# Kernel optimization log

Hardware: AMD Instinct MI355X
Metric: run time of the kernel (lower is better)

Reference implementation:

```python
import jax, jax.numpy as jnp
import numpy as np

N = 100000   # num nodes
E = 1200000  # num edges
D = 64       # embedding dim
K = 3        # propagation hops (alpha has K+1 entries)


def setup_inputs() -> dict:
    key = jax.random.key(0)
    k1, k2, k3 = jax.random.split(key, 3)
    edge_index = jax.random.randint(k1, (2, E), 0, N, dtype=jnp.int64)
    weight = jax.random.normal(k2, (N, D), dtype=jnp.float32)
    alpha = jax.random.uniform(k3, (K + 1,), dtype=jnp.float32)
    return {"edge_index": edge_index, "weight": weight, "alpha": alpha}


def reference(edge_index, weight, alpha):
    row = edge_index[0]  # source j
    col = edge_index[1]  # target i
    # symmetric normalization: in-degree over col, deg^-1/2 with inf -> 0
    deg = jax.ops.segment_sum(jnp.ones((E,), dtype=weight.dtype), col, num_segments=N)
    dinv = jnp.where(deg == 0, 0.0, deg ** -0.5)
    edge_w = dinv[row] * dinv[col]  # [E]

    out = weight * alpha[0]
    x = weight
    for k in range(1, K + 1):
        # gather-scale-scatter propagation hop
        msg = edge_w[:, None] * x[row]                      # [E, D]
        x = jax.ops.segment_sum(msg, col, num_segments=N)   # [N, D]
        out = out + x * alpha[k]

    # per-edge link scores: dot(out[src], out[dst])
    return jnp.sum(out[row] * out[col], axis=-1)  # [E]
```

## Files before the change

kernel.cpp:

```cpp
#include <hip/hip_runtime.h>
#include <hip/hip_bf16.h>

#define GN 100000
#define GE 1200000
#define GD 64
#define NG 256
#define CPG 391
#define CAP 6144


__global__ void detect_kernel(const void* __restrict__ w,
                              const void* __restrict__ edge,
                              int* __restrict__ flags, int* __restrict__ gcount) {
    __shared__ int s_badw, s_edgenz;
    if (threadIdx.x == 0) { s_badw = 0; s_edgenz = 0; }
    gcount[threadIdx.x] = 0;
    __syncthreads();
    const unsigned short* wh = (const unsigned short*)w;
    const unsigned int*   ei = (const unsigned int*)edge;
    int badw = 0, edgenz = 0;
    for (int i = threadIdx.x; i < 4096; i += 256) {
        unsigned int bits = ((unsigned int)wh[i]) << 16;
        float v = __uint_as_float(bits);
        if (!(fabsf(v) <= 100.0f)) badw = 1;
        if ((i & 1) == 1 && ei[i] != 0u) edgenz = 1;
    }
    if (badw)   atomicOr(&s_badw, 1);
    if (edgenz) atomicOr(&s_edgenz, 1);
    __syncthreads();
    if (threadIdx.x == 0) {
        flags[0] = s_badw ? 0 : 1;
        flags[1] = s_edgenz ? 0 : 1;
    }
}

__device__ __forceinline__ int ld_row(const int* __restrict__ edge, int e, int e64) {
    return e64 ? edge[2 * (size_t)e] : edge[e];
}
__device__ __forceinline__ int ld_col(const int* __restrict__ edge, int e, int e64) {
    return e64 ? edge[2 * ((size_t)GE + (size_t)e)] : edge[(size_t)GE + (size_t)e];
}
__device__ __forceinline__ float ld_f(const void* __restrict__ p, size_t i, int bf16f) {
    if (bf16f) return __bfloat162float(((const __hip_bfloat16*)p)[i]);
    return ((const float*)p)[i];
}

__device__ __forceinline__ float bf_lo(unsigned u) { return __uint_as_float(u << 16); }
__device__ __forceinline__ float bf_hi(unsigned u) { return __uint_as_float(u & 0xFFFF0000u); }
__device__ __forceinline__ unsigned bf16bits(float f) {
    __hip_bfloat16 h = __float2bfloat16(f);
    unsigned short s;
    __builtin_memcpy(&s, &h, 2);
    return (unsigned)s;
}

__global__ void p1init_kernel(const int* __restrict__ edge, const int* __restrict__ flags,
                              int* __restrict__ gcount, unsigned* __restrict__ bucket,
                              int E, int chunk,
                              const void* __restrict__ w, const void* __restrict__ alpha,
                              __hip_bfloat16* __restrict__ X,
                              __hip_bfloat16* __restrict__ OUT, int nd) {
    if (blockIdx.x < NG) {
        __shared__ int cnt[NG];
        __shared__ int base[NG];
        int t = threadIdx.x;
        int e64 = flags[1];
        cnt[t] = 0;
        __syncthreads();
        int lo = blockIdx.x * chunk;
        int hiE = min(lo + chunk, E);
        for (int e = lo + t; e < hiE; e += 256) {
            int c = ld_col(edge, e, e64);
            int r = ld_row(edge, e, e64);
            if ((unsigned)c < (unsigned)GN && (unsigned)r < (unsigned)GN)
                atomicAdd(&cnt[c / CPG], 1);
        }
        __syncthreads();
        int cv = cnt[t];
        base[t] = (cv > 0) ? atomicAdd(&gcount[t], cv) : 0;
        __syncthreads();
        cnt[t] = 0;
        __syncthreads();
        for (int e = lo + t; e < hiE; e += 256) {
            int c = ld_col(edge, e, e64);
            int r = ld_row(edge, e, e64);
            if ((unsigned)c < (unsigned)GN && (unsigned)r < (unsigned)GN) {
                int g = c / CPG;
                int idx = base[g] + atomicAdd(&cnt[g], 1);
                if (idx < CAP)
                    bucket[(size_t)g * CAP + idx] = ((unsigned)(c - g * CPG) << 17) | (unsigned)r;
            }
        }
    } else {
        int bid = blockIdx.x - NG;
        int i = 4 * (bid * 256 + (int)threadIdx.x);
        int wbf = flags[0];
        if (i < nd) {
            float a0 = ld_f(alpha, 0, wbf);
            float v0 = ld_f(w, i + 0, wbf);
            float v1 = ld_f(w, i + 1, wbf);
            float v2 = ld_f(w, i + 2, wbf);
            float v3 = ld_f(w, i + 3, wbf);
            uint2 xq;
            xq.x = (bf16bits(v1) << 16) | bf16bits(v0);
            xq.y = (bf16bits(v3) << 16) | bf16bits(v2);
            *(uint2*)(X + i) = xq;
            uint2 oq;
            oq.x = (bf16bits(a0 * v1) << 16) | bf16bits(a0 * v0);
            oq.y = (bf16bits(a0 * v3) << 16) | bf16bits(a0 * v2);
            *(uint2*)(OUT + i) = oq;
        }
    }
}

__global__ void p2_kernel(const unsigned* __restrict__ bucket, const int* __restrict__ gcount,
                          int* __restrict__ rowptr, float* __restrict__ dinv,
                          int* __restrict__ csr) {
    int g = blockIdx.x;
    int t = threadIdx.x;
    __shared__ int gs[NG];
    __shared__ int hist[512];
    __shared__ int s[512];
    int gv = gcount[t]; if (gv > CAP) gv = CAP;
    gs[t] = gv;
    hist[t] = 0; hist[t + 256] = 0;
    __syncthreads();
    for (int off = 1; off < NG; off <<= 1) {
        int u = (t >= off) ? gs[t - off] : 0;
        __syncthreads();
        gs[t] += u;
        __syncthreads();
    }
    int mg = gcount[g]; if (mg > CAP) mg = CAP;
    int gb = gs[g] - mg;
    int m = mg;
    const unsigned* bk = bucket + (size_t)g * CAP;
    for (int idx = t; idx < m; idx += 256)
        atomicAdd(&hist[bk[idx] >> 17], 1);
    __syncthreads();
    int h0 = hist[t], h1 = hist[t + 256];
    s[t] = h0; s[t + 256] = h1;
    __syncthreads();
    for (int off = 1; off < 512; off <<= 1) {
        int v0 = (t >= off) ? s[t - off] : 0;
        int v1 = (t + 256 >= off) ? s[t + 256 - off] : 0;
        __syncthreads();
        s[t] += v0; s[t + 256] += v1;
        __syncthreads();
    }
    int col0 = g * CPG + t;
    int col1 = col0 + 256;
    if (col0 < GN) {
        rowptr[col0] = gb + s[t];
        dinv[col0] = (h0 > 0) ? rsqrtf((float)h0) : 0.0f;
    }
    if (t + 256 < CPG && col1 < GN) {
        rowptr[col1] = gb + s[t + 256];
        dinv[col1] = (h1 > 0) ? rsqrtf((float)h1) : 0.0f;
    }
    __syncthreads();
    hist[t] = s[t] - h0;
    hist[t + 256] = s[t + 256] - h1;
    __syncthreads();
    for (int idx = t; idx < m; idx += 256) {
        unsigned u = bk[idx];
        int cl = u >> 17;
        int r  = (int)(u & 0x1FFFFu);
        int pos = gb + atomicAdd(&hist[cl], 1);
        csr[pos] = r;
    }
}

__global__ void gather_kernel(const __hip_bfloat16* __restrict__ X,
                              __hip_bfloat16* __restrict__ Y,
                              __hip_bfloat16* __restrict__ OUT,
                              const int* __restrict__ rowptr, const int* __restrict__ csr,
                              const float* __restrict__ dinv,
                              const void* __restrict__ alpha, const int* __restrict__ flags,
                              int k, int store_y, int N) {
    int t = blockIdx.x * blockDim.x + threadIdx.x;
    int node = __builtin_amdgcn_readfirstlane(t >> 6);
    if (node >= N) return;
    int lane = t & 63;
    int h = lane >> 4;
    int i = lane & 15;
    int beg = node ? rowptr[node - 1] : 0;
    int end = rowptr[node];
    float dc = dinv[node];
    float a = ld_f(alpha, k, flags[0]);
    size_t obase = (size_t)node * GD + 4 * i;
    uint2 uo = *(const uint2*)(OUT + obase);
    float f0 = 0.0f, f1 = 0.0f, f2 = 0.0f, f3 = 0.0f;
    for (int j = beg; j < end; j += 16) {
        int i0 = j + 0 + h;  int i1 = j + 4 + h;
        int i2 = j + 8 + h;  int i3 = j + 12 + h;
        int last = end - 1;
        int r0 = csr[min(i0, last)];
        int r1 = csr[min(i1, last)];
        int r2 = csr[min(i2, last)];
        int r3 = csr[min(i3, last)];
        float w0 = (i0 < end) ? dinv[r0] : 0.0f;
        float w1 = (i1 < end) ? dinv[r1] : 0.0f;
        float w2 = (i2 < end) ? dinv[r2] : 0.0f;
        float w3 = (i3 < end) ? dinv[r3] : 0.0f;
        uint2 u0 = *(const uint2*)(X + (size_t)r0 * GD + 4 * i);
        uint2 u1 = *(const uint2*)(X + (size_t)r1 * GD + 4 * i);
        uint2 u2 = *(const uint2*)(X + (size_t)r2 * GD + 4 * i);
        uint2 u3 = *(const uint2*)(X + (size_t)r3 * GD + 4 * i);
        f0 = fmaf(w0, bf_lo(u0.x), f0); f1 = fmaf(w0, bf_hi(u0.x), f1);
        f2 = fmaf(w0, bf_lo(u0.y), f2); f3 = fmaf(w0, bf_hi(u0.y), f3);
        f0 = fmaf(w1, bf_lo(u1.x), f0); f1 = fmaf(w1, bf_hi(u1.x), f1);
        f2 = fmaf(w1, bf_lo(u1.y), f2); f3 = fmaf(w1, bf_hi(u1.y), f3);
        f0 = fmaf(w2, bf_lo(u2.x), f0); f1 = fmaf(w2, bf_hi(u2.x), f1);
        f2 = fmaf(w2, bf_lo(u2.y), f2); f3 = fmaf(w2, bf_hi(u2.y), f3);
        f0 = fmaf(w3, bf_lo(u3.x), f0); f1 = fmaf(w3, bf_hi(u3.x), f1);
        f2 = fmaf(w3, bf_lo(u3.y), f2); f3 = fmaf(w3, bf_hi(u3.y), f3);
    }
    f0 += __shfl_xor(f0, 16, 64); f0 += __shfl_xor(f0, 32, 64);
    f1 += __shfl_xor(f1, 16, 64); f1 += __shfl_xor(f1, 32, 64);
    f2 += __shfl_xor(f2, 16, 64); f2 += __shfl_xor(f2, 32, 64);
    f3 += __shfl_xor(f3, 16, 64); f3 += __shfl_xor(f3, 32, 64);
    f0 *= dc; f1 *= dc; f2 *= dc; f3 *= dc;
    if (h == 0) {
        if (store_y) {
            uint2 p;
            p.x = (bf16bits(f1) << 16) | bf16bits(f0);
            p.y = (bf16bits(f3) << 16) | bf16bits(f2);
            *(uint2*)(Y + obase) = p;
        }
        float o0 = fmaf(a, f0, bf_lo(uo.x));
        float o1 = fmaf(a, f1, bf_hi(uo.x));
        float o2 = fmaf(a, f2, bf_lo(uo.y));
        float o3 = fmaf(a, f3, bf_hi(uo.y));
        uint2 q;
        q.x = (bf16bits(o1) << 16) | bf16bits(o0);
        q.y = (bf16bits(o3) << 16) | bf16bits(o2);
        *(uint2*)(OUT + obase) = q;
    }
}

__device__ __forceinline__ float dot2_bf16(unsigned ua, unsigned ub) {
    return fmaf(bf_lo(ua), bf_lo(ub), bf_hi(ua) * bf_hi(ub));
}

__global__ void dot_kernel(const __hip_bfloat16* __restrict__ OUT,
                           const int* __restrict__ edge, const int* __restrict__ flags,
                           void* __restrict__ res, int E) {
    int t = blockIdx.x * blockDim.x + threadIdx.x;
    int e = t >> 2;
    int sub = t & 3;
    if (e >= E) return;
    int e64 = flags[1];
    int wbf = flags[0];
    int r = ld_row(edge, e, e64);
    int c = ld_col(edge, e, e64);
    float p = 0.0f;
    if ((unsigned)r < (unsigned)GN && (unsigned)c < (unsigned)GN) {
        const uint4* pa = (const uint4*)(OUT + (size_t)r * GD + sub * 16);
        const uint4* pb = (const uint4*)(OUT + (size_t)c * GD + sub * 16);
        uint4 a0 = pa[0], a1 = pa[1];
        uint4 b0 = pb[0], b1 = pb[1];
        p = ((dot2_bf16(a0.x, b0.x) + dot2_bf16(a0.y, b0.y)) +
             (dot2_bf16(a0.z, b0.z) + dot2_bf16(a0.w, b0.w))) +
            ((dot2_bf16(a1.x, b1.x) + dot2_bf16(a1.y, b1.y)) +
             (dot2_bf16(a1.z, b1.z) + dot2_bf16(a1.w, b1.w)));
    }
    p += __shfl_down(p, 2, 4);
    p += __shfl_down(p, 1, 4);
    if (sub == 0) {
        if (wbf) ((__hip_bfloat16*)res)[e] = __float2bfloat16(p);
        else     ((float*)res)[e] = p;
    }
}

extern "C" void kernel_launch(void* const* d_in, const int* in_sizes, int n_in,
                              void* d_out, int out_size, void* d_ws, size_t ws_size,
                              hipStream_t stream) {
    const int E = GE, N = GN, ND = GN * GD;

    const void* edge   = d_in[0];
    const void* weight = d_in[1];
    const void* alpha  = d_in[2];

    char* ws = (char*)d_ws;
    int*      flags     = (int*)ws;      ws += 256;
    int*      gcount    = (int*)ws;      ws += 1024;
    float*    dinv      = (float*)ws;    ws += (((size_t)N * 4 + 255) / 256) * 256;
    int*      rowptr    = (int*)ws;      ws += (((size_t)N * 4 + 255) / 256) * 256;
    unsigned* bucket    = (unsigned*)ws; ws += (size_t)NG * CAP * 4;
    int*      csr       = (int*)ws;      ws += (size_t)E * 4;
    __hip_bfloat16* X   = (__hip_bfloat16*)ws; ws += (size_t)ND * 2;
    __hip_bfloat16* Y   = (__hip_bfloat16*)ws; ws += (size_t)ND * 2;
    __hip_bfloat16* OUT = (__hip_bfloat16*)ws; ws += (size_t)ND * 2;

    const int B = 256;

    detect_kernel<<<1, 256, 0, stream>>>(weight, edge, flags, gcount);

    {
        const int chunk = (E + NG - 1) / NG;
        const int initBlocks = (ND / 4 + B - 1) / B;
        p1init_kernel<<<NG + initBlocks, B, 0, stream>>>(
            (const int*)edge, flags, gcount, bucket, E, chunk,
            weight, alpha, X, OUT, ND);
    }
    p2_kernel<<<NG, 256, 0, stream>>>(bucket, gcount, rowptr, dinv, csr);

    const int ggrid = (int)(((size_t)N * 64 + B - 1) / B);
    gather_kernel<<<ggrid, B, 0, stream>>>(X, Y, OUT, rowptr, csr, dinv, alpha, flags, 1, 1, N);
    gather_kernel<<<ggrid, B, 0, stream>>>(Y, X, OUT, rowptr, csr, dinv, alpha, flags, 2, 1, N);
    gather_kernel<<<ggrid, B, 0, stream>>>(X, Y, OUT, rowptr, csr, dinv, alpha, flags, 3, 0, N);

    dot_kernel<<<(int)(((size_t)E * 4 + B - 1) / B), B, 0, stream>>>(OUT, (const int*)edge, flags, d_out, E);
}
```

Baseline: 278.3 us.

## Pre-scale node features by dinv to drop per-edge dinv gathers

Node features are stored pre-multiplied by the source node's dinv, so the gather loop no longer loads dinv[r] for every edge and just sums the neighbour rows. Each hop writes its output scaled by dinv again, so the next hop sees the same pre-scaled form. The initial scaled X is now built inside p2_kernel, where dinv is available in shared memory, instead of in p1init. CSR entries also hold precomputed byte offsets (r<<7) to cut address arithmetic. In exchange, p2 does extra work and rounding order changes slightly, because the scaled values are rounded to bf16.

Measured after the change: 259.3 us. 6.8% less time.

```diff
diff --git a/kernel.cpp b/kernel.cpp
--- a/kernel.cpp
+++ b/kernel.cpp
@@ -58,7 +58,6 @@
                               int* __restrict__ gcount, unsigned* __restrict__ bucket,
                               int E, int chunk,
                               const void* __restrict__ w, const void* __restrict__ alpha,
-                              __hip_bfloat16* __restrict__ X,
                               __hip_bfloat16* __restrict__ OUT, int nd) {
     if (blockIdx.x < NG) {
         __shared__ int cnt[NG];
@@ -101,10 +100,6 @@
             float v1 = ld_f(w, i + 1, wbf);
             float v2 = ld_f(w, i + 2, wbf);
             float v3 = ld_f(w, i + 3, wbf);
-            uint2 xq;
-            xq.x = (bf16bits(v1) << 16) | bf16bits(v0);
-            xq.y = (bf16bits(v3) << 16) | bf16bits(v2);
-            *(uint2*)(X + i) = xq;
             uint2 oq;
             oq.x = (bf16bits(a0 * v1) << 16) | bf16bits(a0 * v0);
             oq.y = (bf16bits(a0 * v3) << 16) | bf16bits(a0 * v2);
@@ -115,12 +110,15 @@
 
 __global__ void p2_kernel(const unsigned* __restrict__ bucket, const int* __restrict__ gcount,
                           int* __restrict__ rowptr, float* __restrict__ dinv,
-                          int* __restrict__ csr) {
+                          int* __restrict__ csr,
+                          const void* __restrict__ w, const int* __restrict__ flags,
+                          __hip_bfloat16* __restrict__ XS) {
     int g = blockIdx.x;
     int t = threadIdx.x;
     __shared__ int gs[NG];
     __shared__ int hist[512];
     __shared__ int s[512];
+    __shared__ float sdv[512];
     int gv = gcount[t]; if (gv > CAP) gv = CAP;
     gs[t] = gv;
     hist[t] = 0; hist[t + 256] = 0;
@@ -148,15 +146,18 @@
         s[t] += v0; s[t + 256] += v1;
         __syncthreads();
     }
+    float dv0 = (h0 > 0) ? rsqrtf((float)h0) : 0.0f;
+    float dv1 = (h1 > 0) ? rsqrtf((float)h1) : 0.0f;
+    sdv[t] = dv0; sdv[t + 256] = dv1;
     int col0 = g * CPG + t;
     int col1 = col0 + 256;
     if (col0 < GN) {
         rowptr[col0] = gb + s[t];
-        dinv[col0] = (h0 > 0) ? rsqrtf((float)h0) : 0.0f;
+        dinv[col0] = dv0;
     }
     if (t + 256 < CPG && col1 < GN) {
         rowptr[col1] = gb + s[t + 256];
-        dinv[col1] = (h1 > 0) ? rsqrtf((float)h1) : 0.0f;
+        dinv[col1] = dv1;
     }
     __syncthreads();
     hist[t] = s[t] - h0;
@@ -167,11 +168,39 @@
         int cl = u >> 17;
         int r  = (int)(u & 0x1FFFFu);
         int pos = gb + atomicAdd(&hist[cl], 1);
-        csr[pos] = r;
-    }
-}
-
-__global__ void gather_kernel(const __hip_bfloat16* __restrict__ X,
+        csr[pos] = r << 7;
+    }
+    int lo = g * CPG;
+    int ncols = min(CPG, GN - lo);
+    int tot = ncols << 6;
+    int wbf = flags[0];
+    size_t gbase = (size_t)lo << 6;
+    if (wbf) {
+        const unsigned short* wp = (const unsigned short*)w;
+        for (int idx = 4 * t; idx < tot; idx += 1024) {
+            float dv = sdv[idx >> 6];
+            size_t base = gbase + (size_t)idx;
+            uint2 wv = *(const uint2*)(wp + base);
+            uint2 o;
+            o.x = (bf16bits(dv * bf_hi(wv.x)) << 16) | bf16bits(dv * bf_lo(wv.x));
+            o.y = (bf16bits(dv * bf_hi(wv.y)) << 16) | bf16bits(dv * bf_lo(wv.y));
+            *(uint2*)(XS + base) = o;
+        }
+    } else {
+        const float* wp = (const float*)w;
+        for (int idx = 4 * t; idx < tot; idx += 1024) {
+            float dv = sdv[idx >> 6];
+            size_t base = gbase + (size_t)idx;
+            float4 wv = *(const float4*)(wp + base);
+            uint2 o;
+            o.x = (bf16bits(dv * wv.y) << 16) | bf16bits(dv * wv.x);
+            o.y = (bf16bits(dv * wv.w) << 16) | bf16bits(dv * wv.z);
+            *(uint2*)(XS + base) = o;
+        }
+    }
+}
+
+__global__ void gather_kernel(const __hip_bfloat16* __restrict__ XS,
                               __hip_bfloat16* __restrict__ Y,
                               __hip_bfloat16* __restrict__ OUT,
                               const int* __restrict__ rowptr, const int* __restrict__ csr,
@@ -190,23 +219,25 @@
     float a = ld_f(alpha, k, flags[0]);
     size_t obase = (size_t)node * GD + 4 * i;
     uint2 uo = *(const uint2*)(OUT + obase);
+    const char* xb = (const char*)XS;
+    unsigned ioff = 8u * (unsigned)i;
+    int last = end - 1;
     float f0 = 0.0f, f1 = 0.0f, f2 = 0.0f, f3 = 0.0f;
     for (int j = beg; j < end; j += 16) {
         int i0 = j + 0 + h;  int i1 = j + 4 + h;
         int i2 = j + 8 + h;  int i3 = j + 12 + h;
-        int last = end - 1;
-        int r0 = csr[min(i0, last)];
-        int r1 = csr[min(i1, last)];
-        int r2 = csr[min(i2, last)];
-        int r3 = csr[min(i3, last)];
-        float w0 = (i0 < end) ? dinv[r0] : 0.0f;
-        float w1 = (i1 < end) ? dinv[r1] : 0.0f;
-        float w2 = (i2 < end) ? dinv[r2] : 0.0f;
-        float w3 = (i3 < end) ? dinv[r3] : 0.0f;
-        uint2 u0 = *(const uint2*)(X + (size_t)r0 * GD + 4 * i);
-        uint2 u1 = *(const uint2*)(X + (size_t)r1 * GD + 4 * i);
-        uint2 u2 = *(const uint2*)(X + (size_t)r2 * GD + 4 * i);
-        uint2 u3 = *(const uint2*)(X + (size_t)r3 * GD + 4 * i);
+        unsigned r0 = (unsigned)csr[min(i0, last)];
+        unsigned r1 = (unsigned)csr[min(i1, last)];
+        unsigned r2 = (unsigned)csr[min(i2, last)];
+        unsigned r3 = (unsigned)csr[min(i3, last)];
+        float w0 = (i0 < end) ? 1.0f : 0.0f;
+        float w1 = (i1 < end) ? 1.0f : 0.0f;
+        float w2 = (i2 < end) ? 1.0f : 0.0f;
+        float w3 = (i3 < end) ? 1.0f : 0.0f;
+        uint2 u0 = *(const uint2*)(xb + (r0 + ioff));
+        uint2 u1 = *(const uint2*)(xb + (r1 + ioff));
+        uint2 u2 = *(const uint2*)(xb + (r2 + ioff));
+        uint2 u3 = *(const uint2*)(xb + (r3 + ioff));
         f0 = fmaf(w0, bf_lo(u0.x), f0); f1 = fmaf(w0, bf_hi(u0.x), f1);
         f2 = fmaf(w0, bf_lo(u0.y), f2); f3 = fmaf(w0, bf_hi(u0.y), f3);
         f0 = fmaf(w1, bf_lo(u1.x), f0); f1 = fmaf(w1, bf_hi(u1.x), f1);
@@ -224,8 +255,8 @@
     if (h == 0) {
         if (store_y) {
             uint2 p;
-            p.x = (bf16bits(f1) << 16) | bf16bits(f0);
-            p.y = (bf16bits(f3) << 16) | bf16bits(f2);
+            p.x = (bf16bits(dc * f1) << 16) | bf16bits(dc * f0);
+            p.y = (bf16bits(dc * f3) << 16) | bf16bits(dc * f2);
             *(uint2*)(Y + obase) = p;
         }
         float o0 = fmaf(a, f0, bf_lo(uo.x));
@@ -302,9 +333,10 @@
         const int initBlocks = (ND / 4 + B - 1) / B;
         p1init_kernel<<<NG + initBlocks, B, 0, stream>>>(
             (const int*)edge, flags, gcount, bucket, E, chunk,
-            weight, alpha, X, OUT, ND);
-    }
-    p2_kernel<<<NG, 256, 0, stream>>>(bucket, gcount, rowptr, dinv, csr);
+            weight, alpha, OUT, ND);
+    }
+    p2_kernel<<<NG, 256, 0, stream>>>(bucket, gcount, rowptr, dinv, csr,
+                                      weight, flags, X);
 
     const int ggrid = (int)(((size_t)N * 64 + B - 1) / B);
     gather_kernel<<<ggrid, B, 0, stream>>>(X, Y, OUT, rowptr, csr, dinv, alpha, flags, 1, 1, N);
```
